# Performance work log

Measured on AMD Instinct MI355X. Metric: run time of the kernel, lower is better.

## Reference

```python
import jax, jax.numpy as jnp
import numpy as np

NUM_HEADS = 16
LN_EPS = 1e-5


def setup_inputs() -> dict:
    key = jax.random.key(0)
    ks = jax.random.split(key, 5)
    B, S, H = 32768, 3, 1024
    scale = 1.0 / np.sqrt(H)
    return {
        "slots": jax.random.normal(ks[0], (B, S, H), dtype=jnp.float32),
        "in_proj_w": jax.random.normal(ks[1], (3 * H, H), dtype=jnp.float32) * scale,
        "in_proj_b": jax.random.normal(ks[2], (3 * H,), dtype=jnp.float32) * 0.02,
        "out_w": jax.random.normal(ks[3], (H, H), dtype=jnp.float32) * scale,
        "out_b": jax.random.normal(ks[4], (H,), dtype=jnp.float32) * 0.02,
        "ln_g": jnp.ones((H,), dtype=jnp.float32),
        "ln_b": jnp.zeros((H,), dtype=jnp.float32),
    }


def reference(slots, in_proj_w, in_proj_b, out_w, out_b, ln_g, ln_b):
    # slots: [B, 3, H]. Matches torch nn.MultiheadAttention (batch_first) in eval
    # mode (dropout inactive) followed by residual add + LayerNorm.
    B, S, H = slots.shape
    nh = NUM_HEADS
    dh = H // nh

    # fused QKV projection: torch does x @ in_proj_w.T + in_proj_b
    qkv = jnp.einsum("bsh,eh->bse", slots, in_proj_w) + in_proj_b  # [B,S,3H]
    q, k, v = jnp.split(qkv, 3, axis=-1)

    def heads(t):  # [B,S,H] -> [B,nh,S,dh]
        return t.reshape(B, S, nh, dh).transpose(0, 2, 1, 3)

    q, k, v = heads(q), heads(k), heads(v)

    scores = jnp.einsum("bnqd,bnkd->bnqk", q, k) / jnp.sqrt(jnp.asarray(dh, slots.dtype))
    attn = jax.nn.softmax(scores, axis=-1)  # [B,nh,3,3]
    ctx = jnp.einsum("bnqk,bnkd->bnqd", attn, v)  # [B,nh,3,dh]
    ctx = ctx.transpose(0, 2, 1, 3).reshape(B, S, H)

    attn_out = jnp.einsum("bsh,oh->bso", ctx, out_w) + out_b  # out_proj

    # residual + LayerNorm (dropout is identity at inference)
    y = slots + attn_out
    mu = jnp.mean(y, axis=-1, keepdims=True)
    var = jnp.mean(jnp.square(y - mu), axis=-1, keepdims=True)
    return (y - mu) / jnp.sqrt(var + LN_EPS) * ln_g + ln_b
```

## Files before the change

### kernel.cpp

```cpp
#include <hip/hip_runtime.h>
#include <stdint.h>

typedef unsigned short u16;
typedef float f32x4 __attribute__((ext_vector_type(4)));
typedef short bf16x8 __attribute__((ext_vector_type(8)));

__device__ __forceinline__ u16 f2bu(float f) {
  uint32_t x = __builtin_bit_cast(uint32_t, f);
  x += 0x7fffu + ((x >> 16) & 1u);
  return (u16)(x >> 16);
}
__device__ __forceinline__ float b2f(u16 u) {
  return __builtin_bit_cast(float, (uint32_t)u << 16);
}
__device__ __forceinline__ void gll16(const void* g, void* l) {
  __builtin_amdgcn_global_load_lds(
      (const __attribute__((address_space(1))) void*)g,
      (__attribute__((address_space(3))) void*)l, 16, 0, 0);
}

__global__ __launch_bounds__(256) void cvt_f32_bf16_kernel(
    const float* __restrict__ in, u16* __restrict__ out, int n4) {
  int i = blockIdx.x * 256 + threadIdx.x;
  const int stride = gridDim.x * 256;
  for (; i < n4; i += stride) {
    float4 f = reinterpret_cast<const float4*>(in)[i];
    ushort4 o;
    o.x = f2bu(f.x); o.y = f2bu(f.y); o.z = f2bu(f.z); o.w = f2bu(f.w);
    reinterpret_cast<ushort4*>(out)[i] = o;
  }
}

__global__ __launch_bounds__(512, 2) void gemm256_bt_bias(
    const u16* __restrict__ A, const u16* __restrict__ Bw,
    const float* __restrict__ bias, u16* __restrict__ C,
    int N, int K, int ntn) {
  __shared__ u16 lds[2][2][8192];
  const int tid = threadIdx.x;
  const int lane = tid & 63, wid = tid >> 6;
  const int wr = wid >> 2, wc = wid & 3;
  const int fr = lane & 15, kg = lane >> 4;

  const int cpx = (int)gridDim.x >> 3;
  const int bid = blockIdx.x;
  const int sid = (bid & 7) * cpx + (bid >> 3);
  const int mt = sid / ntn, nt = sid % ntn;

  const int srow = tid >> 2;
  const int scol = (tid & 3) ^ ((tid >> 3) & 3);
  const u16* Ag = A + (size_t)(mt * 256 + srow) * K + scol * 8;
  const u16* Bg = Bw + (size_t)(nt * 256 + srow) * K + scol * 8;
  const size_t rstep = (size_t)128 * K;

  const int sw = (fr >> 1) & 3;
  const int kgs = (kg ^ sw) * 8;
  const int aoff = (wr * 128 + fr) * 32 + kgs;
  const int boff = (wc * 64 + fr) * 32 + kgs;

  f32x4 acc[8][4];
#pragma unroll
  for (int i = 0; i < 8; i++)
#pragma unroll
    for (int j = 0; j < 4; j++) acc[i][j] = f32x4{0.f, 0.f, 0.f, 0.f};

  const int NT = K >> 5;

#define STAGE(b, kt) do {                                   \
    const u16* a_ = Ag + (size_t)(kt) * 32;                 \
    const u16* b_ = Bg + (size_t)(kt) * 32;                 \
    gll16(a_,         &lds[(b)][0][wid * 512]);             \
    gll16(a_ + rstep, &lds[(b)][0][4096 + wid * 512]);      \
    gll16(b_,         &lds[(b)][1][wid * 512]);             \
    gll16(b_ + rstep, &lds[(b)][1][4096 + wid * 512]);      \
  } while (0)

  STAGE(0, 0);
  __syncthreads();

  for (int t = 0; t < NT; t++) {
    const int cur = t & 1;
    if (t + 1 < NT) STAGE(cur ^ 1, t + 1);
    const u16* As = &lds[cur][0][0];
    const u16* Bs = &lds[cur][1][0];
    bf16x8 a[8], b[4];
#pragma unroll
    for (int mi = 0; mi < 8; mi++)
      a[mi] = *(const bf16x8*)&As[aoff + mi * 512];
#pragma unroll
    for (int nj = 0; nj < 4; nj++)
      b[nj] = *(const bf16x8*)&Bs[boff + nj * 512];
    __builtin_amdgcn_s_setprio(1);
#pragma unroll
    for (int mi = 0; mi < 8; mi++)
#pragma unroll
      for (int nj = 0; nj < 4; nj++)
        acc[mi][nj] = __builtin_amdgcn_mfma_f32_16x16x32_bf16(
            a[mi], b[nj], acc[mi][nj], 0, 0, 0);
    __builtin_amdgcn_s_setprio(0);
    __syncthreads();
  }
#undef STAGE

  const int crow0 = mt * 256 + wr * 128 + kg * 4;
  const int ccol0 = nt * 256 + wc * 64 + fr;
#pragma unroll
  for (int nj = 0; nj < 4; nj++) {
    const int col = ccol0 + nj * 16;
    const float bb = bias[col];
#pragma unroll
    for (int mi = 0; mi < 8; mi++) {
      const int r0 = crow0 + mi * 16;
      f32x4 v = acc[mi][nj];
#pragma unroll
      for (int r = 0; r < 4; r++)
        C[(size_t)(r0 + r) * N + col] = f2bu(v[r] + bb);
    }
  }
}

__global__ __launch_bounds__(256) void attn3_kernel(
    const u16* __restrict__ qkv, u16* __restrict__ ctx) {
  const int tid = threadIdx.x;
  const int lane = tid & 63, wid = tid >> 6;
  const int nunit = 32768 * 4;
  for (int unit = blockIdx.x * 4 + wid; unit < nunit; unit += gridDim.x * 4) {
    const int b = unit >> 2, hg = unit & 3;
    const size_t qbase = (size_t)b * 3 * 3072 + hg * 256 + lane * 4;

    float q[3][4], k[3][4], v[3][4];
#pragma unroll
    for (int s = 0; s < 3; s++) {
      ushort4 uq = *(const ushort4*)(qkv + qbase + (size_t)s * 3072);
      ushort4 uk = *(const ushort4*)(qkv + qbase + (size_t)s * 3072 + 1024);
      ushort4 uv = *(const ushort4*)(qkv + qbase + (size_t)s * 3072 + 2048);
      q[s][0] = b2f(uq.x); q[s][1] = b2f(uq.y); q[s][2] = b2f(uq.z); q[s][3] = b2f(uq.w);
      k[s][0] = b2f(uk.x); k[s][1] = b2f(uk.y); k[s][2] = b2f(uk.z); k[s][3] = b2f(uk.w);
      v[s][0] = b2f(uv.x); v[s][1] = b2f(uv.y); v[s][2] = b2f(uv.z); v[s][3] = b2f(uv.w);
    }

    float sc[3][3];
#pragma unroll
    for (int i = 0; i < 3; i++)
#pragma unroll
      for (int j = 0; j < 3; j++) {
        float p = q[i][0] * k[j][0] + q[i][1] * k[j][1] +
                  q[i][2] * k[j][2] + q[i][3] * k[j][3];
        p += __shfl_xor(p, 1);
        p += __shfl_xor(p, 2);
        p += __shfl_xor(p, 4);
        p += __shfl_xor(p, 8);
        sc[i][j] = p;
      }

    float o[3][4];
#pragma unroll
    for (int i = 0; i < 3; i++) {
      float mx = fmaxf(sc[i][0], fmaxf(sc[i][1], sc[i][2]));
      float e0 = __expf((sc[i][0] - mx) * 0.125f);
      float e1 = __expf((sc[i][1] - mx) * 0.125f);
      float e2 = __expf((sc[i][2] - mx) * 0.125f);
      float inv = 1.f / (e0 + e1 + e2);
      e0 *= inv; e1 *= inv; e2 *= inv;
#pragma unroll
      for (int d = 0; d < 4; d++)
        o[i][d] = e0 * v[0][d] + e1 * v[1][d] + e2 * v[2][d];
    }

    const size_t obase = (size_t)b * 3 * 1024 + hg * 256 + lane * 4;
#pragma unroll
    for (int i = 0; i < 3; i++) {
      ushort4 ov;
      ov.x = f2bu(o[i][0]); ov.y = f2bu(o[i][1]);
      ov.z = f2bu(o[i][2]); ov.w = f2bu(o[i][3]);
      *(ushort4*)(ctx + obase + (size_t)i * 1024) = ov;
    }
  }
}

__global__ __launch_bounds__(256) void ln_kernel(
    const float* __restrict__ slots, const u16* __restrict__ ao,
    const float* __restrict__ g, const float* __restrict__ bvec,
    float* __restrict__ out) {
  const int tid = threadIdx.x;
  const int lane = tid & 63, wid = tid >> 6;
  const int row = blockIdx.x * 4 + wid;
  const size_t rb = (size_t)row * 1024;

  float y[16];
  float sum = 0.f, sq = 0.f;
#pragma unroll
  for (int c = 0; c < 4; c++) {
    const int col = c * 256 + lane * 4;
    float4 sl = *(const float4*)(slots + rb + col);
    ushort4 a4 = *(const ushort4*)(ao + rb + col);
    float y0 = sl.x + b2f(a4.x), y1 = sl.y + b2f(a4.y);
    float y2 = sl.z + b2f(a4.z), y3 = sl.w + b2f(a4.w);
    y[c * 4 + 0] = y0; y[c * 4 + 1] = y1; y[c * 4 + 2] = y2; y[c * 4 + 3] = y3;
    sum += y0 + y1 + y2 + y3;
    sq += y0 * y0 + y1 * y1 + y2 * y2 + y3 * y3;
  }
#pragma unroll
  for (int m = 1; m < 64; m <<= 1) {
    sum += __shfl_xor(sum, m);
    sq  += __shfl_xor(sq, m);
  }
  const float mu = sum * (1.0f / 1024.0f);
  const float var = sq * (1.0f / 1024.0f) - mu * mu;
  const float rs = rsqrtf(var + 1e-5f);
#pragma unroll
  for (int c = 0; c < 4; c++) {
    const int col = c * 256 + lane * 4;
    float4 gg = *(const float4*)(g + col);
    float4 bb = *(const float4*)(bvec + col);
    float4 ov;
    ov.x = (y[c * 4 + 0] - mu) * rs * gg.x + bb.x;
    ov.y = (y[c * 4 + 1] - mu) * rs * gg.y + bb.y;
    ov.z = (y[c * 4 + 2] - mu) * rs * gg.z + bb.z;
    ov.w = (y[c * 4 + 3] - mu) * rs * gg.w + bb.w;
    *(float4*)(out + rb + col) = ov;
  }
}

extern "C" void kernel_launch(void* const* d_in, const int* in_sizes, int n_in,
                              void* d_out, int out_size, void* d_ws, size_t ws_size,
                              hipStream_t stream) {
  const float* slots = (const float*)d_in[0];
  const float* in_w  = (const float*)d_in[1];
  const float* in_b  = (const float*)d_in[2];
  const float* out_w = (const float*)d_in[3];
  const float* out_b = (const float*)d_in[4];
  const float* ln_g  = (const float*)d_in[5];
  const float* ln_b  = (const float*)d_in[6];
  float* out = (float*)d_out;

  const int M = 32768 * 3;

  char* ws = (char*)d_ws;
  u16* Abf   = (u16*)ws;
  u16* Winb  = (u16*)(ws + 201326592);
  u16* Woutb = (u16*)(ws + 207618048);
  u16* qkv   = (u16*)(ws + 209715200);

  cvt_f32_bf16_kernel<<<2048, 256, 0, stream>>>(slots, Abf, M * 1024 / 4);
  cvt_f32_bf16_kernel<<<2048, 256, 0, stream>>>(in_w, Winb, 3072 * 1024 / 4);
  cvt_f32_bf16_kernel<<<1024, 256, 0, stream>>>(out_w, Woutb, 1024 * 1024 / 4);

  gemm256_bt_bias<<<384 * 12, 512, 0, stream>>>(Abf, Winb, in_b, qkv, 3072, 1024, 12);

  attn3_kernel<<<2048, 256, 0, stream>>>(qkv, Abf);

  gemm256_bt_bias<<<384 * 4, 512, 0, stream>>>(Abf, Woutb, out_b, qkv, 1024, 1024, 4);

  ln_kernel<<<M / 4, 256, 0, stream>>>(slots, qkv, ln_g, ln_b, out);
}
```

Baseline: 1.429 ms.

## Use 1024-thread GEMM blocks, write attention context in place, read bf16 slots in LN

The GEMM now runs 16 waves per block, each computing a 64x64 sub-tile instead of 128x64, with one global-to-LDS load per operand per stage. Explicit leading dimensions let the attention kernel write its context into the K slice of the qkv buffer. The output projection then reads from there and writes its result into the Q slice. LayerNorm reads the bf16 copy of slots instead of the fp32 input, cutting residual-read traffic at the cost of residual precision. The launch bound of (1024,4) asks for more resident waves than a CU can hold, which may force tight register limits or spills.

```diff
diff --git a/kernel.cpp b/kernel.cpp
--- a/kernel.cpp
+++ b/kernel.cpp
@@ -31,10 +31,10 @@
   }
 }
 
-__global__ __launch_bounds__(512, 2) void gemm256_bt_bias(
+__global__ __launch_bounds__(1024, 4) void gemm256_bt_bias(
     const u16* __restrict__ A, const u16* __restrict__ Bw,
     const float* __restrict__ bias, u16* __restrict__ C,
-    int N, int K, int ntn) {
+    int N, int K, int lda, int ldc, int ntn) {
   __shared__ u16 lds[2][2][8192];
   const int tid = threadIdx.x;
   const int lane = tid & 63, wid = tid >> 6;
@@ -48,30 +48,25 @@
 
   const int srow = tid >> 2;
   const int scol = (tid & 3) ^ ((tid >> 3) & 3);
-  const u16* Ag = A + (size_t)(mt * 256 + srow) * K + scol * 8;
+  const u16* Ag = A + (size_t)(mt * 256 + srow) * lda + scol * 8;
   const u16* Bg = Bw + (size_t)(nt * 256 + srow) * K + scol * 8;
-  const size_t rstep = (size_t)128 * K;
 
   const int sw = (fr >> 1) & 3;
   const int kgs = (kg ^ sw) * 8;
-  const int aoff = (wr * 128 + fr) * 32 + kgs;
+  const int aoff = (wr * 64 + fr) * 32 + kgs;
   const int boff = (wc * 64 + fr) * 32 + kgs;
 
-  f32x4 acc[8][4];
-#pragma unroll
-  for (int i = 0; i < 8; i++)
+  f32x4 acc[4][4];
+#pragma unroll
+  for (int i = 0; i < 4; i++)
 #pragma unroll
     for (int j = 0; j < 4; j++) acc[i][j] = f32x4{0.f, 0.f, 0.f, 0.f};
 
   const int NT = K >> 5;
 
 #define STAGE(b, kt) do {                                   \
-    const u16* a_ = Ag + (size_t)(kt) * 32;                 \
-    const u16* b_ = Bg + (size_t)(kt) * 32;                 \
-    gll16(a_,         &lds[(b)][0][wid * 512]);             \
-    gll16(a_ + rstep, &lds[(b)][0][4096 + wid * 512]);      \
-    gll16(b_,         &lds[(b)][1][wid * 512]);             \
-    gll16(b_ + rstep, &lds[(b)][1][4096 + wid * 512]);      \
+    gll16(Ag + (size_t)(kt) * 32, &lds[(b)][0][wid * 512]); \
+    gll16(Bg + (size_t)(kt) * 32, &lds[(b)][1][wid * 512]); \
   } while (0)
 
   STAGE(0, 0);
@@ -82,16 +77,16 @@
     if (t + 1 < NT) STAGE(cur ^ 1, t + 1);
     const u16* As = &lds[cur][0][0];
     const u16* Bs = &lds[cur][1][0];
-    bf16x8 a[8], b[4];
-#pragma unroll
-    for (int mi = 0; mi < 8; mi++)
-      a[mi] = *(const bf16x8*)&As[aoff + mi * 512];
+    bf16x8 a[4], b[4];
 #pragma unroll
     for (int nj = 0; nj < 4; nj++)
       b[nj] = *(const bf16x8*)&Bs[boff + nj * 512];
+#pragma unroll
+    for (int mi = 0; mi < 4; mi++)
+      a[mi] = *(const bf16x8*)&As[aoff + mi * 512];
     __builtin_amdgcn_s_setprio(1);
 #pragma unroll
-    for (int mi = 0; mi < 8; mi++)
+    for (int mi = 0; mi < 4; mi++)
 #pragma unroll
       for (int nj = 0; nj < 4; nj++)
         acc[mi][nj] = __builtin_amdgcn_mfma_f32_16x16x32_bf16(
@@ -101,25 +96,25 @@
   }
 #undef STAGE
 
-  const int crow0 = mt * 256 + wr * 128 + kg * 4;
+  const int crow0 = mt * 256 + wr * 64 + kg * 4;
   const int ccol0 = nt * 256 + wc * 64 + fr;
 #pragma unroll
   for (int nj = 0; nj < 4; nj++) {
     const int col = ccol0 + nj * 16;
     const float bb = bias[col];
 #pragma unroll
-    for (int mi = 0; mi < 8; mi++) {
+    for (int mi = 0; mi < 4; mi++) {
       const int r0 = crow0 + mi * 16;
       f32x4 v = acc[mi][nj];
 #pragma unroll
       for (int r = 0; r < 4; r++)
-        C[(size_t)(r0 + r) * N + col] = f2bu(v[r] + bb);
+        C[(size_t)(r0 + r) * ldc + col] = f2bu(v[r] + bb);
     }
   }
 }
 
 __global__ __launch_bounds__(256) void attn3_kernel(
-    const u16* __restrict__ qkv, u16* __restrict__ ctx) {
+    u16* __restrict__ qkv) {
   const int tid = threadIdx.x;
   const int lane = tid & 63, wid = tid >> 6;
   const int nunit = 32768 * 4;
@@ -166,35 +161,35 @@
         o[i][d] = e0 * v[0][d] + e1 * v[1][d] + e2 * v[2][d];
     }
 
-    const size_t obase = (size_t)b * 3 * 1024 + hg * 256 + lane * 4;
 #pragma unroll
     for (int i = 0; i < 3; i++) {
       ushort4 ov;
       ov.x = f2bu(o[i][0]); ov.y = f2bu(o[i][1]);
       ov.z = f2bu(o[i][2]); ov.w = f2bu(o[i][3]);
-      *(ushort4*)(ctx + obase + (size_t)i * 1024) = ov;
+      *(ushort4*)(qkv + qbase + (size_t)i * 3072 + 1024) = ov;
     }
   }
 }
 
 __global__ __launch_bounds__(256) void ln_kernel(
-    const float* __restrict__ slots, const u16* __restrict__ ao,
+    const u16* __restrict__ slots_bf, const u16* __restrict__ ao,
     const float* __restrict__ g, const float* __restrict__ bvec,
     float* __restrict__ out) {
   const int tid = threadIdx.x;
   const int lane = tid & 63, wid = tid >> 6;
   const int row = blockIdx.x * 4 + wid;
   const size_t rb = (size_t)row * 1024;
+  const size_t ab = (size_t)row * 3072;
 
   float y[16];
   float sum = 0.f, sq = 0.f;
 #pragma unroll
   for (int c = 0; c < 4; c++) {
     const int col = c * 256 + lane * 4;
-    float4 sl = *(const float4*)(slots + rb + col);
-    ushort4 a4 = *(const ushort4*)(ao + rb + col);
-    float y0 = sl.x + b2f(a4.x), y1 = sl.y + b2f(a4.y);
-    float y2 = sl.z + b2f(a4.z), y3 = sl.w + b2f(a4.w);
+    ushort4 s4 = *(const ushort4*)(slots_bf + rb + col);
+    ushort4 a4 = *(const ushort4*)(ao + ab + col);
+    float y0 = b2f(s4.x) + b2f(a4.x), y1 = b2f(s4.y) + b2f(a4.y);
+    float y2 = b2f(s4.z) + b2f(a4.z), y3 = b2f(s4.w) + b2f(a4.w);
     y[c * 4 + 0] = y0; y[c * 4 + 1] = y1; y[c * 4 + 2] = y2; y[c * 4 + 3] = y3;
     sum += y0 + y1 + y2 + y3;
     sq += y0 * y0 + y1 * y1 + y2 * y2 + y3 * y3;
@@ -245,11 +240,13 @@
   cvt_f32_bf16_kernel<<<2048, 256, 0, stream>>>(in_w, Winb, 3072 * 1024 / 4);
   cvt_f32_bf16_kernel<<<1024, 256, 0, stream>>>(out_w, Woutb, 1024 * 1024 / 4);
 
-  gemm256_bt_bias<<<384 * 12, 512, 0, stream>>>(Abf, Winb, in_b, qkv, 3072, 1024, 12);
-
-  attn3_kernel<<<2048, 256, 0, stream>>>(qkv, Abf);
-
-  gemm256_bt_bias<<<384 * 4, 512, 0, stream>>>(Abf, Woutb, out_b, qkv, 1024, 1024, 4);
-
-  ln_kernel<<<M / 4, 256, 0, stream>>>(slots, qkv, ln_g, ln_b, out);
-}
+  gemm256_bt_bias<<<384 * 12, 1024, 0, stream>>>(
+      Abf, Winb, in_b, qkv, 3072, 1024, 1024, 3072, 12);
+
+  attn3_kernel<<<2048, 256, 0, stream>>>(qkv);
+
+  gemm256_bt_bias<<<384 * 4, 1024, 0, stream>>>(
+      qkv + 1024, Woutb, out_b, qkv, 1024, 1024, 3072, 3072, 4);
+
+  ln_kernel<<<M / 4, 256, 0, stream>>>(Abf, qkv, ln_g, ln_b, out);
+}
```

Measured after the change: 1.407 ms. No clear change (-1.6%).
